# Kernel tuning notes

Measured on AMD Instinct MI355X. Metric: run time of the kernel, lower is better.

The kernel has to match this reference:

```python
import jax, jax.numpy as jnp
import numpy as np

HIDDEN = 1024
NUM_HEADS = 16
HEAD_DIM = HIDDEN // NUM_HEADS
WINDOW = 512


def setup_inputs() -> dict:
    key = jax.random.key(0)
    ks = jax.random.split(key, 6)
    b, s = 2, 4096
    x = jax.random.normal(ks[0], (b, s, HIDDEN), dtype=jnp.float32)
    attention_mask = jnp.ones((b, s), dtype=jnp.int32)
    scale = 1.0 / np.sqrt(HIDDEN)
    Wq = jax.random.normal(ks[1], (HIDDEN, HIDDEN), dtype=jnp.float32) * scale
    Wk = jax.random.normal(ks[2], (HIDDEN, HIDDEN), dtype=jnp.float32) * scale
    Wv = jax.random.normal(ks[3], (HIDDEN, HIDDEN), dtype=jnp.float32) * scale
    Wo = jax.random.normal(ks[4], (HIDDEN, HIDDEN), dtype=jnp.float32) * scale
    return {"x": x, "attention_mask": attention_mask,
            "Wq": Wq, "Wk": Wk, "Wv": Wv, "Wo": Wo}


def reference(x, attention_mask, Wq, Wk, Wv, Wo):
    b, s, d = x.shape
    # nn.Linear computes x @ W.T
    q = (x @ Wq.T).reshape(b, s, NUM_HEADS, HEAD_DIM).transpose(0, 2, 1, 3)
    k = (x @ Wk.T).reshape(b, s, NUM_HEADS, HEAD_DIM).transpose(0, 2, 1, 3)
    v = (x @ Wv.T).reshape(b, s, NUM_HEADS, HEAD_DIM).transpose(0, 2, 1, 3)
    # [b,h,s,s] scores
    scores = jnp.einsum('bhqd,bhkd->bhqk', q, k) / np.sqrt(HEAD_DIM)
    # causal sliding-window mask: allow j <= i and j >= i - window + 1
    i = jnp.arange(s)[:, None]
    j = jnp.arange(s)[None, :]
    window_mask = (j <= i) & (j >= i - WINDOW + 1)  # [s,s]
    neg_inf = jnp.finfo(scores.dtype).min
    scores = jnp.where(window_mask[None, None], scores, neg_inf)
    pad = attention_mask.astype(bool)[:, None, None, :]  # [b,1,1,s]
    scores = jnp.where(pad, scores, neg_inf)
    probs = jax.nn.softmax(scores, axis=-1)
    out = jnp.einsum('bhqk,bhkd->bhqd', probs, v)
    out = out.transpose(0, 2, 1, 3).reshape(b, s, d)
    return out @ Wo.T
```

## Files before the change

kernel.cpp:

```cpp
#include <hip/hip_runtime.h>
#include <cstdint>
#include <cstddef>

#define HID 1024
#define SEQ 4096
#define NB  2
#define NH  16
#define HD  64
#define WIN 512
#define TOK (NB*SEQ)

typedef _Float16 f16x8 __attribute__((ext_vector_type(8)));
typedef _Float16 f16x4 __attribute__((ext_vector_type(4)));
typedef float    f32x4 __attribute__((ext_vector_type(4)));

__global__ __launch_bounds__(256)
void convertX_kernel(const float* __restrict__ src, _Float16* __restrict__ dst) {
  const int i = (blockIdx.x * 256 + threadIdx.x) * 8;
  f32x4 a = *(const f32x4*)(src + i);
  f32x4 b = *(const f32x4*)(src + i + 4);
  f16x8 o;
#pragma unroll
  for (int r = 0; r < 4; ++r) { o[r] = (_Float16)a[r]; o[r+4] = (_Float16)b[r]; }
  *(f16x8*)(dst + i) = o;
}

__global__ __launch_bounds__(256)
void convertW_kernel(const float* __restrict__ w0, const float* __restrict__ w1,
                     const float* __restrict__ w2, const float* __restrict__ w3,
                     _Float16* __restrict__ dst) {
  const int z = blockIdx.z;
  const float* s = (z == 0) ? w0 : (z == 1) ? w1 : (z == 2) ? w2 : w3;
  _Float16* d = dst + (size_t)z * HID * HID;
  const int i = (blockIdx.x * 256 + threadIdx.x) * 8;
  f32x4 a = *(const f32x4*)(s + i);
  f32x4 b = *(const f32x4*)(s + i + 4);
  f16x8 o;
#pragma unroll
  for (int r = 0; r < 4; ++r) { o[r] = (_Float16)a[r]; o[r+4] = (_Float16)b[r]; }
  *(f16x8*)(d + i) = o;
}

__device__ __forceinline__ void gload16(const void* g, void* lds) {
  __builtin_amdgcn_global_load_lds(
      (__attribute__((address_space(1))) void*)(void*)g,
      (__attribute__((address_space(3))) void*)lds, 16, 0, 0);
}

__device__ __forceinline__ void gemm_mainloop(
    const _Float16* __restrict__ A, const _Float16* __restrict__ W,
    _Float16* sA, _Float16* sB, f32x4 (&acc)[4][4], int m0, int n0) {
  const int tid  = threadIdx.x;
  const int lane = tid & 63;
  const int wave = tid >> 6;
  const int wm = wave >> 1, wn = wave & 1;
  const int l15 = lane & 15, quad = lane >> 4;

  const int o0 = tid * 16;
  const int o1 = o0 + 4096;
  const _Float16* a0 = A + (size_t)(m0 + (o0 >> 6)) * HID + ((o0 & 63) >> 1);
  const _Float16* a1 = A + (size_t)(m0 + (o1 >> 6)) * HID + ((o1 & 63) >> 1);
  const _Float16* w0 = W + (size_t)(n0 + (o0 >> 6)) * HID + ((o0 & 63) >> 1);
  const _Float16* w1 = W + (size_t)(n0 + (o1 >> 6)) * HID + ((o1 & 63) >> 1);
  _Float16* la0 = sA + (o0 >> 1);
  _Float16* la1 = sA + (o1 >> 1);
  _Float16* lb0 = sB + (o0 >> 1);
  _Float16* lb1 = sB + (o1 >> 1);

  const int aoff = (wm*64 + l15)*32 + quad*8;
  const int boff = (wn*64 + l15)*32 + quad*8;

  for (int k0 = 0; k0 < HID; k0 += 64) {
    __syncthreads();
    gload16(a0 + k0,      la0);
    gload16(a1 + k0,      la1);
    gload16(a0 + k0 + 32, la0 + 4096);
    gload16(a1 + k0 + 32, la1 + 4096);
    gload16(w0 + k0,      lb0);
    gload16(w1 + k0,      lb1);
    gload16(w0 + k0 + 32, lb0 + 4096);
    gload16(w1 + k0 + 32, lb1 + 4096);
    __syncthreads();
#pragma unroll
    for (int s = 0; s < 2; ++s) {
      const int sb = s * 4096;
      f16x8 af[4], wf[4];
#pragma unroll
      for (int t = 0; t < 4; ++t) {
        af[t] = *(const f16x8*)(sA + sb + aoff + t*512);
        wf[t] = *(const f16x8*)(sB + sb + boff + t*512);
      }
#pragma unroll
      for (int i = 0; i < 4; ++i)
#pragma unroll
        for (int j = 0; j < 4; ++j)
          acc[i][j] = __builtin_amdgcn_mfma_f32_16x16x32_f16(af[i], wf[j], acc[i][j], 0, 0, 0);
    }
  }
}

__global__ __launch_bounds__(256, 2)
void gemm_qkv_kernel(const _Float16* __restrict__ X,
                     const _Float16* __restrict__ Wh,
                     _Float16* __restrict__ Q,
                     _Float16* __restrict__ Kb,
                     _Float16* __restrict__ Vt) {
  __shared__ __align__(16) _Float16 sA[128*64];
  __shared__ __align__(16) _Float16 sB[128*64];
  const int i = blockIdx.x;
  const int g = i & 7;
  const int j = i >> 3;
  const int c = g*3 + (j >> 6);
  const int z = c % 3;
  const int n0 = (c / 3) * 128;
  const int m0 = (j & 63) * 128;
  const _Float16* W = Wh + (size_t)z * HID * HID;
  f32x4 acc[4][4] = {};
  gemm_mainloop(X, W, sA, sB, acc, m0, n0);

  const int tid  = threadIdx.x;
  const int lane = tid & 63;
  const int wave = tid >> 6;
  const int wm = wave >> 1, wn = wave & 1;
  const int l15 = lane & 15, quad = lane >> 4;

  if (z < 2) {
    _Float16* C = (z == 0) ? Q : Kb;
    const float scl = (z == 0) ? 0.125f : 1.0f;
#pragma unroll
    for (int tm = 0; tm < 4; ++tm)
#pragma unroll
      for (int tn = 0; tn < 4; ++tn) {
        const int row = m0 + wm*64 + tm*16 + quad*4;
        const int col = n0 + wn*64 + tn*16 + l15;
#pragma unroll
        for (int r = 0; r < 4; ++r)
          C[(size_t)(row + r)*HID + col] = (_Float16)(acc[tm][tn][r] * scl);
      }
  } else {
#pragma unroll
    for (int tm = 0; tm < 4; ++tm)
#pragma unroll
      for (int tn = 0; tn < 4; ++tn) {
        const int row = m0 + wm*64 + tm*16 + quad*4;
        const int col = n0 + wn*64 + tn*16 + l15;
        f16x4 v;
#pragma unroll
        for (int r = 0; r < 4; ++r) v[r] = (_Float16)acc[tm][tn][r];
        *(f16x4*)(Vt + (size_t)col*TOK + row) = v;
      }
  }
}

__global__ __launch_bounds__(256, 2)
void gemm_o_kernel(const _Float16* __restrict__ A,
                   const _Float16* __restrict__ Wo,
                   float* __restrict__ C) {
  __shared__ __align__(16) _Float16 sA[128*64];
  __shared__ __align__(16) _Float16 sB[128*64];
  const int i = blockIdx.x;
  const int n0 = (i & 7) * 128;
  const int m0 = (i >> 3) * 128;
  f32x4 acc[4][4] = {};
  gemm_mainloop(A, Wo, sA, sB, acc, m0, n0);

  const int tid  = threadIdx.x;
  const int lane = tid & 63;
  const int wave = tid >> 6;
  const int wm = wave >> 1, wn = wave & 1;
  const int l15 = lane & 15, quad = lane >> 4;
#pragma unroll
  for (int tm = 0; tm < 4; ++tm)
#pragma unroll
    for (int tn = 0; tn < 4; ++tn) {
      const int row = m0 + wm*64 + tm*16 + quad*4;
      const int col = n0 + wn*64 + tn*16 + l15;
#pragma unroll
      for (int r = 0; r < 4; ++r)
        C[(size_t)(row + r)*HID + col] = acc[tm][tn][r];
    }
}

__global__ __launch_bounds__(256, 2)
void attn_kernel(const _Float16* __restrict__ Q, const _Float16* __restrict__ Kb,
                 const _Float16* __restrict__ Vt, const int* __restrict__ AM,
                 _Float16* __restrict__ O) {
  __shared__ __align__(16) _Float16 sK[64*64];
  __shared__ __align__(16) _Float16 sV[64*64];
  __shared__ __align__(16) _Float16 sP[4*32*64];
  __shared__ int sOK;

  const int bi = blockIdx.x;
  const int g  = bi & 7;
  const int jj = bi >> 3;
  const int combo = g*4 + (jj >> 5);
  const int h = combo & 15, b = combo >> 4;
  const int qt = jj & 31;

  const int tid  = threadIdx.x;
  const int lane = tid & 63, wave = tid >> 6;
  const int l15 = lane & 15, quad = lane >> 4;

  const int q0 = qt * 128;
  const int qw = q0 + wave * 32;

  const int swz = l15 & 7;
  const int cA8 = ((quad ^ swz) << 3);
  const int cB8 = (((quad + 4) ^ swz) << 3);

  f16x8 qf[2][2];
#pragma unroll
  for (int ns = 0; ns < 2; ++ns) {
    const size_t qb = (size_t)(b*SEQ + qw + ns*16 + l15)*HID + h*HD + quad*8;
    qf[ns][0] = *(const f16x8*)(Q + qb);
    qf[ns][1] = *(const f16x8*)(Q + qb + 32);
  }

  const int kt_hi = 2*qt + 1;
  int kt_lo = 2*qt - 8; if (kt_lo < 0) kt_lo = 0;

  if (tid == 0) sOK = 1;
  __syncthreads();
  {
    int ok = 1;
    const int jbeg = kt_lo*64, jend = (kt_hi + 1)*64;
    for (int j = jbeg + tid; j < jend; j += 256) ok &= (AM[b*SEQ + j] != 0);
    if (!ok) sOK = 0;
  }
  __syncthreads();
  const bool allok = (sOK != 0);

  const int prow = tid >> 3;
  const int pc   = tid & 7;
  const int pco  = ((pc ^ (prow & 7)) << 3);
  f16x8 pk0, pk1, pv0, pv1;
  {
    const int j0 = kt_lo * 64;
    const _Float16* kp = Kb + (size_t)(b*SEQ + j0 + prow)*HID + h*HD + pco;
    pk0 = *(const f16x8*)kp;
    pk1 = *(const f16x8*)(kp + (size_t)32*HID);
    const _Float16* vp = Vt + (size_t)(h*HD + prow)*TOK + b*SEQ + j0 + pco;
    pv0 = *(const f16x8*)vp;
    pv1 = *(const f16x8*)(vp + (size_t)32*TOK);
  }

  float m_run[2] = {-1e20f, -1e20f}, l_run[2] = {0.0f, 0.0f};
  f32x4 o[4][2] = {};
  _Float16* myP = sP + wave * (32*64);

  for (int kt = kt_lo; kt <= kt_hi; ++kt) {
    const int j0 = kt * 64;
    __syncthreads();
    *(f16x8*)(sK + tid*8)        = pk0;
    *(f16x8*)(sK + tid*8 + 2048) = pk1;
    *(f16x8*)(sV + tid*8)        = pv0;
    *(f16x8*)(sV + tid*8 + 2048) = pv1;
    __syncthreads();
    if (kt < kt_hi) {
      int jn = (kt + 1) * 64; if (jn > SEQ - 64) jn = SEQ - 64;
      const _Float16* kp = Kb + (size_t)(b*SEQ + jn + prow)*HID + h*HD + pco;
      pk0 = *(const f16x8*)kp;
      pk1 = *(const f16x8*)(kp + (size_t)32*HID);
      const _Float16* vp = Vt + (size_t)(h*HD + prow)*TOK + b*SEQ + jn + pco;
      pv0 = *(const f16x8*)vp;
      pv1 = *(const f16x8*)(vp + (size_t)32*TOK);
    }

    f32x4 sc[4][2] = {};
#pragma unroll
    for (int t = 0; t < 4; ++t) {
      const f16x8 kf0 = *(const f16x8*)(sK + (t*16 + l15)*64 + cA8);
      const f16x8 kf1 = *(const f16x8*)(sK + (t*16 + l15)*64 + cB8);
      sc[t][0] = __builtin_amdgcn_mfma_f32_16x16x32_f16(kf0, qf[0][0], sc[t][0], 0, 0, 0);
      sc[t][0] = __builtin_amdgcn_mfma_f32_16x16x32_f16(kf1, qf[0][1], sc[t][0], 0, 0, 0);
      sc[t][1] = __builtin_amdgcn_mfma_f32_16x16x32_f16(kf0, qf[1][0], sc[t][1], 0, 0, 0);
      sc[t][1] = __builtin_amdgcn_mfma_f32_16x16x32_f16(kf1, qf[1][1], sc[t][1], 0, 0, 0);
    }

    if (!allok) {
#pragma unroll
      for (int t = 0; t < 4; ++t)
#pragma unroll
        for (int r = 0; r < 4; ++r) {
          const float ad = (AM[b*SEQ + j0 + t*16 + quad*4 + r] == 0) ? -2e30f : 0.0f;
          sc[t][0][r] += ad;
          sc[t][1][r] += ad;
        }
    }

#pragma unroll
    for (int ns = 0; ns < 2; ++ns) {
      const int i = qw + ns*16 + l15;
      float mx = -1e30f;
#pragma unroll
      for (int t = 0; t < 4; ++t)
#pragma unroll
        for (int r = 0; r < 4; ++r) {
          const int j = j0 + t*16 + quad*4 + r;
          const bool valid = (unsigned)(i - j) < WIN;
          const float s = valid ? sc[t][ns][r] : -1e30f;
          sc[t][ns][r] = s;
          mx = fmaxf(mx, s);
        }
      mx = fmaxf(mx, __shfl_xor(mx, 16, 64));
      mx = fmaxf(mx, __shfl_xor(mx, 32, 64));
      const float mnew = fmaxf(m_run[ns], mx);
      const float alpha = __expf(m_run[ns] - mnew);
      m_run[ns] = mnew;
      float sum = 0.0f;
#pragma unroll
      for (int t = 0; t < 4; ++t) {
        f16x4 pv;
#pragma unroll
        for (int r = 0; r < 4; ++r) {
          const float p = __expf(sc[t][ns][r] - mnew);
          sum += p;
          pv[r] = (_Float16)p;
        }
        const int paddr = (ns*16 + l15)*64 + (((2*t + (quad >> 1)) ^ swz) << 3) + (quad & 1)*4;
        *(f16x4*)(myP + paddr) = pv;
      }
      sum += __shfl_xor(sum, 16, 64);
      sum += __shfl_xor(sum, 32, 64);
      l_run[ns] = l_run[ns]*alpha + sum;
#pragma unroll
      for (int dt = 0; dt < 4; ++dt)
#pragma unroll
        for (int r = 0; r < 4; ++r) o[dt][ns][r] *= alpha;
    }

    const f16x8 pf00 = *(const f16x8*)(myP + l15*64 + cA8);
    const f16x8 pf01 = *(const f16x8*)(myP + l15*64 + cB8);
    const f16x8 pf10 = *(const f16x8*)(myP + (16 + l15)*64 + cA8);
    const f16x8 pf11 = *(const f16x8*)(myP + (16 + l15)*64 + cB8);
#pragma unroll
    for (int dt = 0; dt < 4; ++dt) {
      const f16x8 vf0 = *(const f16x8*)(sV + (dt*16 + l15)*64 + cA8);
      const f16x8 vf1 = *(const f16x8*)(sV + (dt*16 + l15)*64 + cB8);
      o[dt][0] = __builtin_amdgcn_mfma_f32_16x16x32_f16(vf0, pf00, o[dt][0], 0, 0, 0);
      o[dt][0] = __builtin_amdgcn_mfma_f32_16x16x32_f16(vf1, pf01, o[dt][0], 0, 0, 0);
      o[dt][1] = __builtin_amdgcn_mfma_f32_16x16x32_f16(vf0, pf10, o[dt][1], 0, 0, 0);
      o[dt][1] = __builtin_amdgcn_mfma_f32_16x16x32_f16(vf1, pf11, o[dt][1], 0, 0, 0);
    }
  }

  const float inv[2] = {1.0f / fmaxf(l_run[0], 1e-30f), 1.0f / fmaxf(l_run[1], 1e-30f)};
#pragma unroll
  for (int ns = 0; ns < 2; ++ns) {
    const size_t ob = (size_t)(b*SEQ + qw + ns*16 + l15)*HID + h*HD + quad*4;
#pragma unroll
    for (int dt = 0; dt < 4; ++dt) {
      f16x4 v;
#pragma unroll
      for (int r = 0; r < 4; ++r) v[r] = (_Float16)(o[dt][ns][r] * inv[ns]);
      *(f16x4*)(O + ob + dt*16) = v;
    }
  }
}

extern "C" void kernel_launch(void* const* d_in, const int* in_sizes, int n_in,
                              void* d_out, int out_size, void* d_ws, size_t ws_size,
                              hipStream_t stream) {
  const float* X  = (const float*)d_in[0];
  const int*   AM = (const int*)d_in[1];
  const float* Wq = (const float*)d_in[2];
  const float* Wk = (const float*)d_in[3];
  const float* Wv = (const float*)d_in[4];
  const float* Wo = (const float*)d_in[5];
  float* out = (float*)d_out;

  _Float16* Xh = (_Float16*)d_ws;
  _Float16* Wh = Xh + (size_t)TOK*HID;
  _Float16* Qb = Wh + (size_t)4*HID*HID;
  _Float16* Kb = Qb + (size_t)TOK*HID;
  _Float16* Vt = Kb + (size_t)TOK*HID;
  _Float16* AO = Vt + (size_t)TOK*HID;

  dim3 blk(256);
  convertX_kernel<<<dim3((TOK*HID)/(256*8)), blk, 0, stream>>>(X, Xh);
  convertW_kernel<<<dim3((HID*HID)/(256*8), 1, 4), blk, 0, stream>>>(Wq, Wk, Wv, Wo, Wh);
  gemm_qkv_kernel<<<dim3(1536), blk, 0, stream>>>(Xh, Wh, Qb, Kb, Vt);
  attn_kernel<<<dim3(1024), blk, 0, stream>>>(Qb, Kb, Vt, AM, AO);
  gemm_o_kernel<<<dim3(512), blk, 0, stream>>>(AO, Wh + (size_t)3*HID*HID, out);
}
```

Baseline: 241.6 us.

## Merge conversion kernels, remap GEMM block order, raise occupancy bounds

Folds the X and weight fp32-to-fp16 conversions into one launch to save a kernel launch. Remaps block indices in the QKV and output GEMMs so consecutive blocks on each XCD share M tiles and sweep N, aiming for better L2 reuse. Raises the launch_bounds minimum blocks per CU to 3 for the GEMMs and 4 for attention. The tighter bounds can force register spills.

```diff
diff --git a/kernel.cpp b/kernel.cpp
--- a/kernel.cpp
+++ b/kernel.cpp
@@ -15,30 +15,27 @@
 typedef float    f32x4 __attribute__((ext_vector_type(4)));
 
 __global__ __launch_bounds__(256)
-void convertX_kernel(const float* __restrict__ src, _Float16* __restrict__ dst) {
-  const int i = (blockIdx.x * 256 + threadIdx.x) * 8;
+void convert_kernel(const float* __restrict__ X, const float* __restrict__ w0,
+                    const float* __restrict__ w1, const float* __restrict__ w2,
+                    const float* __restrict__ w3,
+                    _Float16* __restrict__ Xh, _Float16* __restrict__ Wh) {
+  const int bi = blockIdx.x;
+  const float* src; _Float16* dst; size_t off;
+  if (bi < 4096) {
+    src = X; dst = Xh; off = (size_t)bi * 2048;
+  } else {
+    const int wi = bi - 4096, z = wi >> 9;
+    src = (z == 0) ? w0 : (z == 1) ? w1 : (z == 2) ? w2 : w3;
+    dst = Wh + (size_t)z * HID * HID;
+    off = (size_t)(wi & 511) * 2048;
+  }
+  const size_t i = off + (size_t)threadIdx.x * 8;
   f32x4 a = *(const f32x4*)(src + i);
   f32x4 b = *(const f32x4*)(src + i + 4);
   f16x8 o;
 #pragma unroll
   for (int r = 0; r < 4; ++r) { o[r] = (_Float16)a[r]; o[r+4] = (_Float16)b[r]; }
   *(f16x8*)(dst + i) = o;
-}
-
-__global__ __launch_bounds__(256)
-void convertW_kernel(const float* __restrict__ w0, const float* __restrict__ w1,
-                     const float* __restrict__ w2, const float* __restrict__ w3,
-                     _Float16* __restrict__ dst) {
-  const int z = blockIdx.z;
-  const float* s = (z == 0) ? w0 : (z == 1) ? w1 : (z == 2) ? w2 : w3;
-  _Float16* d = dst + (size_t)z * HID * HID;
-  const int i = (blockIdx.x * 256 + threadIdx.x) * 8;
-  f32x4 a = *(const f32x4*)(s + i);
-  f32x4 b = *(const f32x4*)(s + i + 4);
-  f16x8 o;
-#pragma unroll
-  for (int r = 0; r < 4; ++r) { o[r] = (_Float16)a[r]; o[r+4] = (_Float16)b[r]; }
-  *(f16x8*)(d + i) = o;
 }
 
 __device__ __forceinline__ void gload16(const void* g, void* lds) {
@@ -99,7 +96,7 @@
   }
 }
 
-__global__ __launch_bounds__(256, 2)
+__global__ __launch_bounds__(256, 3)
 void gemm_qkv_kernel(const _Float16* __restrict__ X,
                      const _Float16* __restrict__ Wh,
                      _Float16* __restrict__ Q,
@@ -107,13 +104,14 @@
                      _Float16* __restrict__ Vt) {
   __shared__ __align__(16) _Float16 sA[128*64];
   __shared__ __align__(16) _Float16 sB[128*64];
-  const int i = blockIdx.x;
-  const int g = i & 7;
-  const int j = i >> 3;
-  const int c = g*3 + (j >> 6);
-  const int z = c % 3;
-  const int n0 = (c / 3) * 128;
-  const int m0 = (j & 63) * 128;
+  const int i  = blockIdx.x;
+  const int g  = i & 7;
+  const int j  = i >> 3;
+  const int mi = j & 7;
+  const int c  = j >> 3;
+  const int z  = c >> 3;
+  const int n0 = (c & 7) * 128;
+  const int m0 = (g*8 + mi) * 128;
   const _Float16* W = Wh + (size_t)z * HID * HID;
   f32x4 acc[4][4] = {};
   gemm_mainloop(X, W, sA, sB, acc, m0, n0);
@@ -152,15 +150,18 @@
   }
 }
 
-__global__ __launch_bounds__(256, 2)
+__global__ __launch_bounds__(256, 3)
 void gemm_o_kernel(const _Float16* __restrict__ A,
                    const _Float16* __restrict__ Wo,
                    float* __restrict__ C) {
   __shared__ __align__(16) _Float16 sA[128*64];
   __shared__ __align__(16) _Float16 sB[128*64];
-  const int i = blockIdx.x;
-  const int n0 = (i & 7) * 128;
-  const int m0 = (i >> 3) * 128;
+  const int i  = blockIdx.x;
+  const int g  = i & 7;
+  const int j  = i >> 3;
+  const int mi = j & 7;
+  const int n0 = (j >> 3) * 128;
+  const int m0 = (g*8 + mi) * 128;
   f32x4 acc[4][4] = {};
   gemm_mainloop(A, Wo, sA, sB, acc, m0, n0);
 
@@ -181,7 +182,7 @@
     }
 }
 
-__global__ __launch_bounds__(256, 2)
+__global__ __launch_bounds__(256, 4)
 void attn_kernel(const _Float16* __restrict__ Q, const _Float16* __restrict__ Kb,
                  const _Float16* __restrict__ Vt, const int* __restrict__ AM,
                  _Float16* __restrict__ O) {
@@ -377,8 +378,7 @@
   _Float16* AO = Vt + (size_t)TOK*HID;
 
   dim3 blk(256);
-  convertX_kernel<<<dim3((TOK*HID)/(256*8)), blk, 0, stream>>>(X, Xh);
-  convertW_kernel<<<dim3((HID*HID)/(256*8), 1, 4), blk, 0, stream>>>(Wq, Wk, Wv, Wo, Wh);
+  convert_kernel<<<dim3(4096 + 4*512), blk, 0, stream>>>(X, Wq, Wk, Wv, Wo, Xh, Wh);
   gemm_qkv_kernel<<<dim3(1536), blk, 0, stream>>>(Xh, Wh, Qb, Kb, Vt);
   attn_kernel<<<dim3(1024), blk, 0, stream>>>(Qb, Kb, Vt, AM, AO);
   gemm_o_kernel<<<dim3(512), blk, 0, stream>>>(AO, Wh + (size_t)3*HID*HID, out);
```

New measurement: 255.8 us. 5.9% more time.
